# Kernel tuning notes

Hardware: AMD Instinct MI355X
Metric: run time of the kernel (lower is better)

Reference implementation:

```python
import jax, jax.numpy as jnp
import numpy as np
from jax import lax

NMS_THRESHOLD = 0.7
POST_NMS_TOP_N = 1000
N_BOXES = 2048
CAP = 8  # max vertices of intersection of two convex quads
EPS = 1e-8


def _cross(a, b):
    return a[..., 0] * b[..., 1] - a[..., 1] * b[..., 0]


def _corners(b):
    # b: (5,) [xc, yc, w, h, theta] -> (4,2) CCW corners
    xc, yc, w, h, t = b[0], b[1], b[2], b[3], b[4]
    c, s = jnp.cos(t), jnp.sin(t)
    lx = jnp.array([-0.5, 0.5, 0.5, -0.5], dtype=b.dtype) * w
    ly = jnp.array([-0.5, -0.5, 0.5, 0.5], dtype=b.dtype) * h
    x = xc + lx * c - ly * s
    y = yc + lx * s + ly * c
    return jnp.stack([x, y], axis=-1)


def _clip(poly, n, p0, p1):
    # Sutherland-Hodgman clip of poly (CAP,2) with n valid verts against
    # half-plane to the left of edge p0->p1 (CCW interior).
    idx = jnp.arange(CAP)
    valid = idx < n
    nsafe = jnp.maximum(n, 1)
    prev = poly[(idx + nsafe - 1) % nsafe]
    e = p1 - p0
    d_cur = _cross(e, poly - p0)
    d_prev = _cross(e, prev - p0)
    cur_in = d_cur >= 0.0
    prev_in = d_prev >= 0.0
    denom = d_prev - d_cur
    denom = jnp.where(jnp.abs(denom) < EPS, EPS, denom)
    t = d_prev / denom
    ipt = prev + t[:, None] * (poly - prev)  # edge/half-plane intersection
    # per input vertex emit: [crossing point, current vertex]
    pts = jnp.stack([ipt, poly], axis=1).reshape(2 * CAP, 2)
    vmask = jnp.stack([valid & (cur_in != prev_in), valid & cur_in], axis=1).reshape(2 * CAP)
    order = jnp.argsort(~vmask, stable=True)  # compact valid points to front
    new_n = jnp.minimum(jnp.sum(vmask).astype(jnp.int32), CAP)
    return pts[order][:CAP], new_n


def _inter_area(b1, b2):
    poly = jnp.zeros((CAP, 2), dtype=b1.dtype).at[:4].set(_corners(b1))
    n = jnp.int32(4)
    r2 = _corners(b2)
    for k in range(4):
        poly, n = _clip(poly, n, r2[k], r2[(k + 1) % 4])
    idx = jnp.arange(CAP)
    valid = idx < n
    nxt = (idx + 1) % jnp.maximum(n, 1)
    area = 0.5 * jnp.abs(jnp.sum(jnp.where(valid, _cross(poly, poly[nxt]), 0.0)))
    return jnp.where(n >= 3, area, 0.0)


def _pairwise_iou(boxes):
    inter = jax.vmap(lambda b1: jax.vmap(lambda b2: _inter_area(b1, b2))(boxes))(boxes)
    area = boxes[:, 2] * boxes[:, 3]
    return inter / (area[:, None] + area[None, :] - inter + EPS)


def _greedy(iou, thresh, topn):
    n = iou.shape[0]
    js = jnp.arange(n, dtype=jnp.int32)

    def body(i, st):
        keep, cnt, sup = st
        take = jnp.logical_and(jnp.logical_not(sup[i]), cnt < topn)
        keep = jnp.where(take, keep.at[cnt].set(i), keep)
        sup = sup | (take & (iou[i] >= thresh) & (js > i))
        return keep, cnt + take.astype(jnp.int32), sup

    keep0 = jnp.full((topn,), -1, dtype=jnp.int32)
    keep, _, _ = lax.fori_loop(0, n, body, (keep0, jnp.int32(0), jnp.zeros((n,), dtype=bool)))
    return keep


def setup_inputs() -> dict:
    key = jax.random.key(0)
    k1, k2, k3 = jax.random.split(key, 3)
    xy = jax.random.uniform(k1, (N_BOXES, 2), minval=0.0, maxval=1024.0)
    wh = jax.random.uniform(k2, (N_BOXES, 2), minval=8.0, maxval=128.0)
    th = jax.random.uniform(k3, (N_BOXES, 1), minval=-np.pi / 2, maxval=np.pi / 2)
    r_boxes = jnp.concatenate([xy, wh, th], axis=1).astype(jnp.float32)
    return {"r_boxes": r_boxes}


def reference(r_boxes):
    # boxes assumed pre-sorted by score (as in the original module)
    iou = _pairwise_iou(r_boxes)
    keep = _greedy(iou, NMS_THRESHOLD, POST_NMS_TOP_N)  # (post_nms_top_n,), -1 padded
    return keep
```

## Files before the change

### kernel.cpp

```cpp
#include <hip/hip_runtime.h>
#include <hip/hip_bf16.h>

#define CAP 8
#define EPSF 1e-8f
#define NMS_THR 0.7f
#define TOPN 1000
#define ITILE 16
#define QCAP (256 * ITILE)
#define PCAP 8192
#define CAPR 64
#define SCRATCH_ROWS 512

__device__ __forceinline__ float rect_inter_area_cs(
    float xc1, float yc1, float w1, float h1, float c1, float s1,
    float xc2, float yc2, float w2, float h2, float c2, float s2)
{
    float px[CAP], py[CAP];
    {
        float lx0 = -0.5f * w1, lx1 = 0.5f * w1;
        float ly0 = -0.5f * h1, ly1 = 0.5f * h1;
        px[0] = xc1 + lx0 * c1 - ly0 * s1;  py[0] = yc1 + lx0 * s1 + ly0 * c1;
        px[1] = xc1 + lx1 * c1 - ly0 * s1;  py[1] = yc1 + lx1 * s1 + ly0 * c1;
        px[2] = xc1 + lx1 * c1 - ly1 * s1;  py[2] = yc1 + lx1 * s1 + ly1 * c1;
        px[3] = xc1 + lx0 * c1 - ly1 * s1;  py[3] = yc1 + lx0 * s1 + ly1 * c1;
#pragma unroll
        for (int s2i = 4; s2i < CAP; ++s2i) { px[s2i] = 0.f; py[s2i] = 0.f; }
    }
    float qx[4], qy[4];
    {
        float lx0 = -0.5f * w2, lx1 = 0.5f * w2;
        float ly0 = -0.5f * h2, ly1 = 0.5f * h2;
        qx[0] = xc2 + lx0 * c2 - ly0 * s2;  qy[0] = yc2 + lx0 * s2 + ly0 * c2;
        qx[1] = xc2 + lx1 * c2 - ly0 * s2;  qy[1] = yc2 + lx1 * s2 + ly0 * c2;
        qx[2] = xc2 + lx1 * c2 - ly1 * s2;  qy[2] = yc2 + lx1 * s2 + ly1 * c2;
        qx[3] = xc2 + lx0 * c2 - ly1 * s2;  qy[3] = yc2 + lx0 * s2 + ly1 * c2;
    }

    int n = 4;
#pragma unroll
    for (int e = 0; e < 4; ++e) {
        float p0x = qx[e], p0y = qy[e];
        float ex = qx[(e + 1) & 3] - p0x, ey = qy[(e + 1) & 3] - p0y;

        float pxp = px[0], pyp = py[0];
#pragma unroll
        for (int s = 1; s < CAP; ++s)
            if (s == n - 1) { pxp = px[s]; pyp = py[s]; }
        float dp = ex * (pyp - p0y) - ey * (pxp - p0x);

        float nx_[CAP], ny_[CAP];
#pragma unroll
        for (int s = 0; s < CAP; ++s) { nx_[s] = 0.f; ny_[s] = 0.f; }
        int m = 0;

#pragma unroll
        for (int k = 0; k < CAP; ++k) {
            bool act = (k < n);
            float pxc = px[k], pyc = py[k];
            float dc = ex * (pyc - p0y) - ey * (pxc - p0x);
            bool cin = (dc >= 0.0f), pin = (dp >= 0.0f);

            float den = dp - dc;
            den = (fabsf(den) < EPSF) ? EPSF : den;
            float t = dp / den;
            float ix = pxp + t * (pxc - pxp);
            float iy = pyp + t * (pyc - pyp);

            bool emit_cross = act && (cin != pin);
            if (emit_cross) {
#pragma unroll
                for (int s = 0; s < CAP; ++s)
                    if (s == m) { nx_[s] = ix; ny_[s] = iy; }
                ++m;
            }
            bool emit_cur = act && cin;
            if (emit_cur) {
#pragma unroll
                for (int s = 0; s < CAP; ++s)
                    if (s == m) { nx_[s] = pxc; ny_[s] = pyc; }
                ++m;
            }
            if (act) { pxp = pxc; pyp = pyc; dp = dc; }
        }
        n = (m < CAP) ? m : CAP;
#pragma unroll
        for (int s = 0; s < CAP; ++s) { px[s] = nx_[s]; py[s] = ny_[s]; }
    }

    if (n < 3) return 0.0f;
    float s = 0.0f;
#pragma unroll
    for (int k = 0; k < CAP; ++k) {
        if (k < n) {
            float nxk = px[(k + 1) & (CAP - 1)];
            float nyk = py[(k + 1) & (CAP - 1)];
            if (k == n - 1) { nxk = px[0]; nyk = py[0]; }
            s += px[k] * nyk - py[k] * nxk;
        }
    }
    return 0.5f * fabsf(s);
}

__device__ __forceinline__ unsigned long long rl64(unsigned long long v, int l) {
    unsigned int lo = (unsigned int)__builtin_amdgcn_readlane((int)(unsigned int)v, l);
    unsigned int hi = (unsigned int)__builtin_amdgcn_readlane((int)(v >> 32), l);
    return ((unsigned long long)hi << 32) | lo;
}

__global__ __launch_bounds__(256)
void filter_kernel(const float* __restrict__ boxes,
                   unsigned int* __restrict__ cnt_per_block,
                   unsigned int* __restrict__ pairs, int slice, int n)
{
    __shared__ float4 atile[2 * ITILE];
    __shared__ unsigned int q[QCAP];
    __shared__ int qcnt, scnt;

    const int tid = threadIdx.x;
    const int bid = blockIdx.x;

    const int itiles = (n + ITILE - 1) / ITILE;
    const int jtiles = (n + 255) / 256;
    int L2 = bid, jt = -1, it = 0;
    for (int q2 = 0; q2 < jtiles; ++q2) {
        int c2 = (q2 * 256 + 254) / ITILE + 1;
        c2 = (c2 < itiles) ? c2 : itiles;
        if (jt < 0) {
            if (L2 < c2) { jt = q2; it = L2; }
            else L2 -= c2;
        }
    }
    const int i0 = it * ITILE;
    const int j = jt * 256 + tid;

    if (tid == 0) { qcnt = 0; scnt = 0; }
    if (tid < ITILE) {
        int i = i0 + tid;
        if (i < n) {
            const float* b = boxes + (size_t)i * 5;
            float x = b[0], y = b[1], w = b[2], h = b[3], th = b[4];
            atile[2 * tid]     = make_float4(x, y, w, h);
            atile[2 * tid + 1] = make_float4(cosf(th), sinf(th),
                                             0.5f * sqrtf(w * w + h * h), w * h);
        } else {
            atile[2 * tid]     = make_float4(0.f, 0.f, 0.f, 0.f);
            atile[2 * tid + 1] = make_float4(0.f, 0.f, 0.f, 0.f);
        }
    }
    __syncthreads();

    float4 B0, B1;
    bool jok = (j < n);
    if (jok) {
        const float* b = boxes + (size_t)j * 5;
        float x = b[0], y = b[1], w = b[2], h = b[3], th = b[4];
        B0 = make_float4(x, y, w, h);
        B1 = make_float4(cosf(th), sinf(th),
                         0.5f * sqrtf(w * w + h * h), w * h);
    } else { B0 = make_float4(0,0,0,0); B1 = make_float4(0,0,0,0); }

#pragma unroll
    for (int ii = 0; ii < ITILE; ++ii) {
        int i = i0 + ii;
        float4 A0 = atile[2 * ii], A1 = atile[2 * ii + 1];
        bool pass = jok && (j > i) && (i < n);
        float dx = A0.x - B0.x, dy = A0.y - B0.y;
        float rr = A1.z + B1.z + 1e-2f;
        pass = pass && (dx * dx + dy * dy <= rr * rr);
        float amin = fminf(A1.w, B1.w), amax = fmaxf(A1.w, B1.w);
        pass = pass && (amin >= 0.699f * amax);
        if (pass) {
            int idx = atomicAdd(&qcnt, 1);
            q[idx] = ((unsigned int)ii << 16) | (unsigned int)j;
        }
    }
    __syncthreads();

    int qn = qcnt;
    for (int t = tid; t < qn; t += 256) {
        unsigned int pk = q[t];
        int ii = (int)(pk >> 16), j2 = (int)(pk & 0xffffu);
        int i2 = i0 + ii;
        float4 A0 = atile[2 * ii], A1 = atile[2 * ii + 1];
        const float* b = boxes + (size_t)j2 * 5;
        float x = b[0], y = b[1], w = b[2], h = b[3], th = b[4];
        float cj = cosf(th), sj = sinf(th);
        float a1 = A1.w, a2 = w * h;
        float inter = rect_inter_area_cs(A0.x, A0.y, A0.z, A0.w, A1.x, A1.y,
                                         x, y, w, h, cj, sj);
        float iou = inter / (a1 + a2 - inter + EPSF);
        if (iou >= NMS_THR) {
            int s2 = atomicAdd(&scnt, 1);
            if (s2 < slice)
                pairs[(size_t)bid * slice + s2] =
                    ((unsigned int)i2 << 16) | (unsigned int)j2;
        }
    }
    __syncthreads();

    if (tid == 0)
        cnt_per_block[bid] = (unsigned int)((scnt < slice) ? scnt : slice);
}

__global__ __launch_bounds__(256, 1)
void greedy_kernel(const unsigned int* __restrict__ cnt_per_block,
                   const unsigned int* __restrict__ pairs, int slice,
                   unsigned int* __restrict__ scratch32,
                   int* __restrict__ keep, int n, int T)
{
    __shared__ unsigned int plist[PCAP];
    __shared__ unsigned int rowdat32[CAPR * 64];
    __shared__ unsigned int szv32[64];
    __shared__ int bexcl_lds[32];
    __shared__ int Rtot, pcnt, ovf;

    const int tid = threadIdx.x;
    const int chunks = (n + 63) >> 6;

    if (tid == 0) { pcnt = 0; ovf = 0; }
    for (int t = tid; t < 64; t += 256) szv32[t] = 0u;
    __syncthreads();

    for (int b = tid; b < T; b += 256) {
        int cb = (int)cnt_per_block[b];
        if (cb > slice) cb = slice;
        for (int t2 = 0; t2 < cb; ++t2) {
            unsigned int p = pairs[(size_t)b * slice + t2];
            int idx = atomicAdd(&pcnt, 1);
            if (idx < PCAP) plist[idx] = p;
            else ovf = 1;
        }
    }
    __syncthreads();
    int np = (pcnt < PCAP) ? pcnt : PCAP;

    for (int t = tid; t < np; t += 256) {
        int i = (int)(plist[t] >> 16);
        atomicOr(&szv32[((i >> 6) << 1) + ((i >> 5) & 1)], 1u << (i & 31));
    }
    if (ovf) {
        for (int b = tid; b < T; b += 256) {
            int cb = (int)cnt_per_block[b];
            if (cb > slice) cb = slice;
            for (int t2 = 0; t2 < cb; ++t2) {
                unsigned int p = pairs[(size_t)b * slice + t2];
                int i = (int)(p >> 16);
                atomicOr(&szv32[((i >> 6) << 1) + ((i >> 5) & 1)],
                         1u << (i & 31));
            }
        }
    }
    __syncthreads();

    if (tid < 64) {
        int lane = tid;
        unsigned long long szv = (lane < chunks)
            ? ((unsigned long long)szv32[2 * lane] |
               ((unsigned long long)szv32[2 * lane + 1] << 32)) : 0ULL;
        int pc = __popcll(szv);
        int pref = pc;
#pragma unroll
        for (int d = 1; d < 64; d <<= 1) {
            int t = __shfl_up(pref, d);
            if (lane >= d) pref += t;
        }
        if (lane < chunks) bexcl_lds[lane] = pref - pc;
        if (lane == chunks - 1) Rtot = pref;
    }
    __syncthreads();

    int R = Rtot;
    int Rc = (R < CAPR) ? R : CAPR;
    int Rs = ((R < CAPR + SCRATCH_ROWS) ? R : (CAPR + SCRATCH_ROWS)) - Rc;
    for (int t = tid; t < Rc * 64; t += 256) rowdat32[t] = 0u;
    for (int t = tid; t < Rs * 64; t += 256) scratch32[t] = 0u;
    __syncthreads();

    auto scatter = [&](unsigned int p) {
        int i = (int)(p >> 16), jj = (int)(p & 0xffffu);
        int c = i >> 6;
        unsigned long long szc =
            (unsigned long long)szv32[2 * c] |
            ((unsigned long long)szv32[2 * c + 1] << 32);
        int slot = bexcl_lds[c] +
            (int)__popcll(szc & (((i & 63) == 0) ? 0ULL
                                 : ((~0ULL) >> (64 - (i & 63)))));
        if (slot < CAPR)
            atomicOr(&rowdat32[slot * 64 + (jj >> 5)], 1u << (jj & 31));
        else if (slot < CAPR + SCRATCH_ROWS)
            atomicOr(&scratch32[(slot - CAPR) * 64 + (jj >> 5)],
                     1u << (jj & 31));
    };
    for (int t = tid; t < np; t += 256) scatter(plist[t]);
    if (ovf) {
        for (int b = tid; b < T; b += 256) {
            int cb = (int)cnt_per_block[b];
            if (cb > slice) cb = slice;
            for (int t2 = 0; t2 < cb; ++t2)
                scatter(pairs[(size_t)b * slice + t2]);
        }
    }
    __syncthreads();

    if (tid >= 64) return;
    {
        const int lane = tid;
        unsigned long long szv = (lane < chunks)
            ? ((unsigned long long)szv32[2 * lane] |
               ((unsigned long long)szv32[2 * lane + 1] << 32)) : 0ULL;
        int base_excl = (lane < chunks) ? bexcl_lds[lane] : 0;

        auto rowread = [&](int slot, int word) -> unsigned long long {
            if (slot < CAPR)
                return (unsigned long long)rowdat32[slot * 64 + 2 * word] |
                       ((unsigned long long)rowdat32[slot * 64 + 2 * word + 1]
                        << 32);
            if (slot < CAPR + SCRATCH_ROWS)
                return (unsigned long long)
                           scratch32[(slot - CAPR) * 64 + 2 * word] |
                       ((unsigned long long)
                           scratch32[(slot - CAPR) * 64 + 2 * word + 1] << 32);
            return 0ULL;
        };

        unsigned long long acc = 0ULL;
        int cnt = 0;

        for (int c = 0; c < chunks; ++c) {
            if (cnt >= TOPN) break;
            const int base = c << 6;
            unsigned long long cw = rl64(acc, c);
            unsigned long long nzc = rl64(szv, c);
            unsigned long long valid =
                (n - base >= 64) ? ~0ULL : ((1ULL << (n - base)) - 1ULL);
            unsigned long long cand = ~cw & valid;
            int rem = TOPN - cnt;

            unsigned long long kmask;
            if ((nzc & cand) == 0ULL && __popcll(cand) <= rem) {
                kmask = cand;
            } else {
                int bexc = __builtin_amdgcn_readlane(base_excl, c);
                unsigned long long D = 0ULL;
                if ((nzc >> lane) & 1ULL) {
                    int slot = bexc +
                        (int)__popcll(nzc & ((lane == 0) ? 0ULL
                                             : ((~0ULL) >> (64 - lane))));
                    D = rowread(slot, c);
                }
                unsigned long long intra = __ballot((D & cand) != 0ULL);
                if ((intra & cand) == 0ULL && __popcll(cand) <= rem) {
                    kmask = cand;
                } else {
                    kmask = 0ULL;
                    int cl = cnt;
#pragma unroll
                    for (int k = 0; k < 64; ++k) {
                        if (!((cw >> k) & 1ULL) && cl < TOPN && (base + k) < n) {
                            cw |= rl64(D, k);
                            kmask |= (1ULL << k);
                            ++cl;
                        }
                    }
                }
            }

            if ((kmask >> lane) & 1ULL)
                keep[cnt + __popcll(kmask & ((1ULL << lane) - 1ULL))] =
                    base + lane;
            cnt += __popcll(kmask);

            unsigned long long orrows = kmask & nzc;
            if (orrows) {
                int bexc = __builtin_amdgcn_readlane(base_excl, c);
                while (orrows) {
                    int r = (int)__builtin_ctzll(orrows);
                    orrows &= orrows - 1ULL;
                    int slot = bexc +
                        (int)__popcll(nzc & ((r == 0) ? 0ULL
                                             : ((~0ULL) >> (64 - r))));
                    acc |= rowread(slot, lane & 31);
                }
            }
        }

        for (int t = cnt + lane; t < TOPN; t += 64) keep[t] = -1;
    }
}

extern "C" void kernel_launch(void* const* d_in, const int* in_sizes, int n_in,
                              void* d_out, int out_size, void* d_ws, size_t ws_size,
                              hipStream_t stream) {
    const float* boxes = (const float*)d_in[0];
    int n = in_sizes[0] / 5;
    int* keep = (int*)d_out;

    const int itiles = (n + ITILE - 1) / ITILE;
    const int jtiles = (n + 255) / 256;
    int T = 0;
    for (int q2 = 0; q2 < jtiles; ++q2) {
        int c2 = (q2 * 256 + 254) / ITILE + 1;
        T += (c2 < itiles) ? c2 : itiles;
    }

    unsigned int* cnt_per_block = (unsigned int*)d_ws;
    size_t off_pairs = (((size_t)T * 4) + 255) & ~(size_t)255;
    size_t fixed_tail = (size_t)SCRATCH_ROWS * 256 + 256;
    long avail = (long)ws_size - (long)off_pairs - (long)fixed_tail;
    int slice = QCAP;
    long maxslice = avail / ((long)T * 4);
    if (slice > maxslice) slice = (int)maxslice;
    unsigned int* pairs = (unsigned int*)((char*)d_ws + off_pairs);
    unsigned int* scratch32 = pairs + (size_t)T * slice;

    filter_kernel<<<T, 256, 0, stream>>>(boxes, cnt_per_block, pairs, slice, n);
    greedy_kernel<<<1, 256, 0, stream>>>(cnt_per_block, pairs, slice,
                                         scratch32, keep, n, T);
}
```

Before: 26.38 us.

## Fuse filter and greedy kernels via last-block-done atomic counter

Merges the pair-filter kernel and the single-block greedy NMS kernel into one launch. Each block does its filtering work, then bumps a global done counter with acquire-release semantics, and the last block to finish runs the greedy pass. Cross-block reads of pairs and counts go through relaxed agent-scope atomic loads and stores. This removes the second kernel launch and its gap, but adds a memset launch to reset the counter, and every block now allocates the larger shared-memory footprint of the greedy stage, which may lower occupancy in the filter phase.

```diff
diff --git a/kernel.cpp b/kernel.cpp
--- a/kernel.cpp
+++ b/kernel.cpp
@@ -10,6 +10,13 @@
 #define PCAP 8192
 #define CAPR 64
 #define SCRATCH_ROWS 512
+
+__device__ __forceinline__ void gstore(unsigned int* p, unsigned int v) {
+    __hip_atomic_store(p, v, __ATOMIC_RELAXED, __HIP_MEMORY_SCOPE_AGENT);
+}
+__device__ __forceinline__ unsigned int gload(const unsigned int* p) {
+    return __hip_atomic_load(p, __ATOMIC_RELAXED, __HIP_MEMORY_SCOPE_AGENT);
+}
 
 __device__ __forceinline__ float rect_inter_area_cs(
     float xc1, float yc1, float w1, float h1, float c1, float s1,
@@ -108,124 +115,126 @@
 }
 
 __global__ __launch_bounds__(256)
-void filter_kernel(const float* __restrict__ boxes,
-                   unsigned int* __restrict__ cnt_per_block,
-                   unsigned int* __restrict__ pairs, int slice, int n)
-{
-    __shared__ float4 atile[2 * ITILE];
-    __shared__ unsigned int q[QCAP];
-    __shared__ int qcnt, scnt;
-
-    const int tid = threadIdx.x;
-    const int bid = blockIdx.x;
-
-    const int itiles = (n + ITILE - 1) / ITILE;
-    const int jtiles = (n + 255) / 256;
-    int L2 = bid, jt = -1, it = 0;
-    for (int q2 = 0; q2 < jtiles; ++q2) {
-        int c2 = (q2 * 256 + 254) / ITILE + 1;
-        c2 = (c2 < itiles) ? c2 : itiles;
-        if (jt < 0) {
-            if (L2 < c2) { jt = q2; it = L2; }
-            else L2 -= c2;
-        }
-    }
-    const int i0 = it * ITILE;
-    const int j = jt * 256 + tid;
-
-    if (tid == 0) { qcnt = 0; scnt = 0; }
-    if (tid < ITILE) {
-        int i = i0 + tid;
-        if (i < n) {
-            const float* b = boxes + (size_t)i * 5;
-            float x = b[0], y = b[1], w = b[2], h = b[3], th = b[4];
-            atile[2 * tid]     = make_float4(x, y, w, h);
-            atile[2 * tid + 1] = make_float4(cosf(th), sinf(th),
-                                             0.5f * sqrtf(w * w + h * h), w * h);
-        } else {
-            atile[2 * tid]     = make_float4(0.f, 0.f, 0.f, 0.f);
-            atile[2 * tid + 1] = make_float4(0.f, 0.f, 0.f, 0.f);
-        }
-    }
-    __syncthreads();
-
-    float4 B0, B1;
-    bool jok = (j < n);
-    if (jok) {
-        const float* b = boxes + (size_t)j * 5;
-        float x = b[0], y = b[1], w = b[2], h = b[3], th = b[4];
-        B0 = make_float4(x, y, w, h);
-        B1 = make_float4(cosf(th), sinf(th),
-                         0.5f * sqrtf(w * w + h * h), w * h);
-    } else { B0 = make_float4(0,0,0,0); B1 = make_float4(0,0,0,0); }
-
-#pragma unroll
-    for (int ii = 0; ii < ITILE; ++ii) {
-        int i = i0 + ii;
-        float4 A0 = atile[2 * ii], A1 = atile[2 * ii + 1];
-        bool pass = jok && (j > i) && (i < n);
-        float dx = A0.x - B0.x, dy = A0.y - B0.y;
-        float rr = A1.z + B1.z + 1e-2f;
-        pass = pass && (dx * dx + dy * dy <= rr * rr);
-        float amin = fminf(A1.w, B1.w), amax = fmaxf(A1.w, B1.w);
-        pass = pass && (amin >= 0.699f * amax);
-        if (pass) {
-            int idx = atomicAdd(&qcnt, 1);
-            q[idx] = ((unsigned int)ii << 16) | (unsigned int)j;
-        }
-    }
-    __syncthreads();
-
-    int qn = qcnt;
-    for (int t = tid; t < qn; t += 256) {
-        unsigned int pk = q[t];
-        int ii = (int)(pk >> 16), j2 = (int)(pk & 0xffffu);
-        int i2 = i0 + ii;
-        float4 A0 = atile[2 * ii], A1 = atile[2 * ii + 1];
-        const float* b = boxes + (size_t)j2 * 5;
-        float x = b[0], y = b[1], w = b[2], h = b[3], th = b[4];
-        float cj = cosf(th), sj = sinf(th);
-        float a1 = A1.w, a2 = w * h;
-        float inter = rect_inter_area_cs(A0.x, A0.y, A0.z, A0.w, A1.x, A1.y,
-                                         x, y, w, h, cj, sj);
-        float iou = inter / (a1 + a2 - inter + EPSF);
-        if (iou >= NMS_THR) {
-            int s2 = atomicAdd(&scnt, 1);
-            if (s2 < slice)
-                pairs[(size_t)bid * slice + s2] =
-                    ((unsigned int)i2 << 16) | (unsigned int)j2;
-        }
-    }
-    __syncthreads();
-
-    if (tid == 0)
-        cnt_per_block[bid] = (unsigned int)((scnt < slice) ? scnt : slice);
-}
-
-__global__ __launch_bounds__(256, 1)
-void greedy_kernel(const unsigned int* __restrict__ cnt_per_block,
-                   const unsigned int* __restrict__ pairs, int slice,
-                   unsigned int* __restrict__ scratch32,
-                   int* __restrict__ keep, int n, int T)
+void fused_kernel(const float* __restrict__ boxes,
+                  unsigned int* __restrict__ done,
+                  unsigned int* __restrict__ cnt_per_block,
+                  unsigned int* __restrict__ pairs, int slice,
+                  unsigned int* __restrict__ scratch32,
+                  int* __restrict__ keep, int n, int T)
 {
     __shared__ unsigned int plist[PCAP];
+    __shared__ float4 atile[2 * ITILE];
     __shared__ unsigned int rowdat32[CAPR * 64];
     __shared__ unsigned int szv32[64];
     __shared__ int bexcl_lds[32];
-    __shared__ int Rtot, pcnt, ovf;
+    __shared__ int qcnt, scnt, Rtot, pcnt, ovf, lastflag;
 
     const int tid = threadIdx.x;
+    const int bid = blockIdx.x;
     const int chunks = (n + 63) >> 6;
+
+    {
+        const int itiles = (n + ITILE - 1) / ITILE;
+        const int jtiles = (n + 255) / 256;
+        int L2 = bid, jt = -1, it = 0;
+        for (int q2 = 0; q2 < jtiles; ++q2) {
+            int c2 = (q2 * 256 + 254) / ITILE + 1;
+            c2 = (c2 < itiles) ? c2 : itiles;
+            if (jt < 0) {
+                if (L2 < c2) { jt = q2; it = L2; }
+                else L2 -= c2;
+            }
+        }
+        const int i0 = it * ITILE;
+        const int j = jt * 256 + tid;
+
+        if (tid == 0) { qcnt = 0; scnt = 0; }
+        if (tid < ITILE) {
+            int i = i0 + tid;
+            if (i < n) {
+                const float* b = boxes + (size_t)i * 5;
+                float x = b[0], y = b[1], w = b[2], h = b[3], th = b[4];
+                atile[2 * tid]     = make_float4(x, y, w, h);
+                atile[2 * tid + 1] = make_float4(
+                    cosf(th), sinf(th), 0.5f * sqrtf(w * w + h * h), w * h);
+            } else {
+                atile[2 * tid]     = make_float4(0.f, 0.f, 0.f, 0.f);
+                atile[2 * tid + 1] = make_float4(0.f, 0.f, 0.f, 0.f);
+            }
+        }
+        __syncthreads();
+
+        float4 B0, B1;
+        bool jok = (j < n);
+        if (jok) {
+            const float* b = boxes + (size_t)j * 5;
+            float x = b[0], y = b[1], w = b[2], h = b[3], th = b[4];
+            B0 = make_float4(x, y, w, h);
+            B1 = make_float4(cosf(th), sinf(th),
+                             0.5f * sqrtf(w * w + h * h), w * h);
+        } else { B0 = make_float4(0,0,0,0); B1 = make_float4(0,0,0,0); }
+
+#pragma unroll
+        for (int ii = 0; ii < ITILE; ++ii) {
+            int i = i0 + ii;
+            float4 A0 = atile[2 * ii], A1 = atile[2 * ii + 1];
+            bool pass = jok && (j > i) && (i < n);
+            float dx = A0.x - B0.x, dy = A0.y - B0.y;
+            float rr = A1.z + B1.z + 1e-2f;
+            pass = pass && (dx * dx + dy * dy <= rr * rr);
+            float amin = fminf(A1.w, B1.w), amax = fmaxf(A1.w, B1.w);
+            pass = pass && (amin >= 0.699f * amax);
+            if (pass) {
+                int idx = atomicAdd(&qcnt, 1);
+                plist[idx] = ((unsigned int)ii << 16) | (unsigned int)j;
+            }
+        }
+        __syncthreads();
+
+        int qn = qcnt;
+        for (int t = tid; t < qn; t += 256) {
+            unsigned int pk = plist[t];
+            int ii = (int)(pk >> 16), j2 = (int)(pk & 0xffffu);
+            int i2 = i0 + ii;
+            float4 A0 = atile[2 * ii], A1 = atile[2 * ii + 1];
+            const float* b = boxes + (size_t)j2 * 5;
+            float x = b[0], y = b[1], w = b[2], h = b[3], th = b[4];
+            float cj = cosf(th), sj = sinf(th);
+            float a1 = A1.w, a2 = w * h;
+            float inter = rect_inter_area_cs(
+                A0.x, A0.y, A0.z, A0.w, A1.x, A1.y, x, y, w, h, cj, sj);
+            float iou = inter / (a1 + a2 - inter + EPSF);
+            if (iou >= NMS_THR) {
+                int s2 = atomicAdd(&scnt, 1);
+                if (s2 < slice)
+                    gstore(&pairs[(size_t)bid * slice + s2],
+                           ((unsigned int)i2 << 16) | (unsigned int)j2);
+            }
+        }
+        __syncthreads();
+
+        if (tid == 0)
+            gstore(&cnt_per_block[bid],
+                   (unsigned int)((scnt < slice) ? scnt : slice));
+    }
+
+    if (tid == 0) {
+        unsigned int old = __hip_atomic_fetch_add(done, 1u, __ATOMIC_ACQ_REL,
+                                                  __HIP_MEMORY_SCOPE_AGENT);
+        lastflag = (old == (unsigned int)(T - 1));
+    }
+    __syncthreads();
+    if (!lastflag) return;
 
     if (tid == 0) { pcnt = 0; ovf = 0; }
     for (int t = tid; t < 64; t += 256) szv32[t] = 0u;
     __syncthreads();
 
     for (int b = tid; b < T; b += 256) {
-        int cb = (int)cnt_per_block[b];
+        int cb = (int)gload(&cnt_per_block[b]);
         if (cb > slice) cb = slice;
         for (int t2 = 0; t2 < cb; ++t2) {
-            unsigned int p = pairs[(size_t)b * slice + t2];
+            unsigned int p = gload(&pairs[(size_t)b * slice + t2]);
             int idx = atomicAdd(&pcnt, 1);
             if (idx < PCAP) plist[idx] = p;
             else ovf = 1;
@@ -240,10 +249,10 @@
     }
     if (ovf) {
         for (int b = tid; b < T; b += 256) {
-            int cb = (int)cnt_per_block[b];
+            int cb = (int)gload(&cnt_per_block[b]);
             if (cb > slice) cb = slice;
             for (int t2 = 0; t2 < cb; ++t2) {
-                unsigned int p = pairs[(size_t)b * slice + t2];
+                unsigned int p = gload(&pairs[(size_t)b * slice + t2]);
                 int i = (int)(p >> 16);
                 atomicOr(&szv32[((i >> 6) << 1) + ((i >> 5) & 1)],
                          1u << (i & 31));
@@ -294,10 +303,10 @@
     for (int t = tid; t < np; t += 256) scatter(plist[t]);
     if (ovf) {
         for (int b = tid; b < T; b += 256) {
-            int cb = (int)cnt_per_block[b];
+            int cb = (int)gload(&cnt_per_block[b]);
             if (cb > slice) cb = slice;
             for (int t2 = 0; t2 < cb; ++t2)
-                scatter(pairs[(size_t)b * slice + t2]);
+                scatter(gload(&pairs[(size_t)b * slice + t2]));
         }
     }
     __syncthreads();
@@ -403,8 +412,9 @@
         T += (c2 < itiles) ? c2 : itiles;
     }
 
-    unsigned int* cnt_per_block = (unsigned int*)d_ws;
-    size_t off_pairs = (((size_t)T * 4) + 255) & ~(size_t)255;
+    unsigned int* done = (unsigned int*)d_ws;
+    unsigned int* cnt_per_block = done + 64;
+    size_t off_pairs = (256 + (size_t)T * 4 + 255) & ~(size_t)255;
     size_t fixed_tail = (size_t)SCRATCH_ROWS * 256 + 256;
     long avail = (long)ws_size - (long)off_pairs - (long)fixed_tail;
     int slice = QCAP;
@@ -413,7 +423,8 @@
     unsigned int* pairs = (unsigned int*)((char*)d_ws + off_pairs);
     unsigned int* scratch32 = pairs + (size_t)T * slice;
 
-    filter_kernel<<<T, 256, 0, stream>>>(boxes, cnt_per_block, pairs, slice, n);
-    greedy_kernel<<<1, 256, 0, stream>>>(cnt_per_block, pairs, slice,
-                                         scratch32, keep, n, T);
-}
+    hipMemsetAsync(done, 0, 16, stream);
+
+    fused_kernel<<<T, 256, 0, stream>>>(boxes, done, cnt_per_block, pairs,
+                                        slice, scratch32, keep, n, T);
+}
```

After: 36.39 us. 38.0% more time.
